# Kernel optimization log

Hardware: AMD Instinct MI355X
Metric: run time of the kernel (lower is better)

The kernel has to match this reference:

```python
import jax, jax.numpy as jnp
import numpy as np

N = 50000        # nodes
E = 800000       # directed edges (before self-loops)
F_IN = 128       # input node features
HID = 32         # hidden channels per head
HEADS = 4
NCLS = 8
EPS_BN = 1e-5
NEG_SLOPE = 0.2  # GATConv LeakyReLU default


def setup_inputs() -> dict:
    key = jax.random.key(0)
    ks = jax.random.split(key, 16)
    rn = lambda k, shape, s=0.1: jax.random.normal(k, shape, jnp.float32) * s
    inp = {}
    inp["x"] = jax.random.normal(ks[0], (N, F_IN), jnp.float32)
    inp["edge_index"] = jax.random.randint(ks[1], (2, E), 0, N, dtype=jnp.int32)
    # layer 0: F_IN -> HEADS*HID (concat)
    inp["W0"] = rn(ks[2], (F_IN, HEADS * HID))
    inp["as0"] = rn(ks[3], (HEADS, HID))
    inp["ad0"] = rn(ks[4], (HEADS, HID))
    inp["b0"] = jnp.zeros((HEADS * HID,), jnp.float32)
    inp["g0"] = jnp.ones((HEADS * HID,), jnp.float32)
    inp["bb0"] = jnp.zeros((HEADS * HID,), jnp.float32)
    inp["rm0"] = jnp.zeros((HEADS * HID,), jnp.float32)
    inp["rv0"] = jnp.ones((HEADS * HID,), jnp.float32)
    # layer 1: HEADS*HID -> HEADS*HID (concat)
    inp["W1"] = rn(ks[5], (HEADS * HID, HEADS * HID))
    inp["as1"] = rn(ks[6], (HEADS, HID))
    inp["ad1"] = rn(ks[7], (HEADS, HID))
    inp["b1"] = jnp.zeros((HEADS * HID,), jnp.float32)
    inp["g1"] = jnp.ones((HEADS * HID,), jnp.float32)
    inp["bb1"] = jnp.zeros((HEADS * HID,), jnp.float32)
    inp["rm1"] = jnp.zeros((HEADS * HID,), jnp.float32)
    inp["rv1"] = jnp.ones((HEADS * HID,), jnp.float32)
    # layer 2: HEADS*HID -> NCLS, heads=1, concat=False
    inp["W2"] = rn(ks[8], (HEADS * HID, NCLS))
    inp["as2"] = rn(ks[9], (1, NCLS))
    inp["ad2"] = rn(ks[10], (1, NCLS))
    inp["b2"] = jnp.zeros((NCLS,), jnp.float32)
    return inp


def gat_conv(x, src, dst, W, att_s, att_d, bias, H, C, concat):
    """PyG-style GATConv (eval mode, self-loops already appended to src/dst)."""
    n = x.shape[0]
    h = (x @ W).reshape(n, H, C)                       # [N,H,C]
    a_s = (h * att_s).sum(-1)                          # [N,H]
    a_d = (h * att_d).sum(-1)                          # [N,H]
    e = jax.nn.leaky_relu(a_s[src] + a_d[dst], NEG_SLOPE)  # [E,H]
    # numerically-stable segment softmax over incoming edges of each dst node
    m = jax.ops.segment_max(e, dst, num_segments=n)
    m = jnp.where(jnp.isfinite(m), m, 0.0)
    ex = jnp.exp(e - m[dst])
    den = jax.ops.segment_sum(ex, dst, num_segments=n)
    alpha = ex / (den[dst] + 1e-16)                    # [E,H]
    out = jax.ops.segment_sum(h[src] * alpha[:, :, None], dst, num_segments=n)  # [N,H,C]
    out = out.reshape(n, H * C) if concat else out.mean(axis=1)
    return out + bias


def bn_eval(x, g, b, rm, rv):
    return (x - rm) * jax.lax.rsqrt(rv + EPS_BN) * g + b


def reference(x, edge_index, W0, as0, ad0, b0, g0, bb0, rm0, rv0,
              W1, as1, ad1, b1, g1, bb1, rm1, rv1, W2, as2, ad2, b2):
    n = x.shape[0]
    loop = jnp.arange(n, dtype=edge_index.dtype)       # self-loops (PyG default)
    src = jnp.concatenate([edge_index[0], loop])
    dst = jnp.concatenate([edge_index[1], loop])
    h = gat_conv(x, src, dst, W0, as0, ad0, b0, HEADS, HID, True)
    h = jax.nn.elu(bn_eval(h, g0, bb0, rm0, rv0))
    h = gat_conv(h, src, dst, W1, as1, ad1, b1, HEADS, HID, True)
    h = jax.nn.elu(bn_eval(h, g1, bb1, rm1, rv1))
    h = gat_conv(h, src, dst, W2, as2, ad2, b2, 1, NCLS, False)
    return jax.nn.log_softmax(h, axis=1)
```

## Files before the change

### kernel.cpp

```cpp
#include <hip/hip_runtime.h>
#include <math.h>

#define N_NODES 50000
#define N_EDGES 800000
#define ET (N_EDGES + N_NODES)
#define FDIM 128
#define HEADS 4
#define HID 32
#define NCLS 8
#define NEG 0.2f
#define EPS_BN 1e-5f

#define BSH 6
#define NBUCK ((N_NODES + 63) >> BSH)
#define EPB 4096

typedef __attribute__((ext_vector_type(8))) short short8;
typedef __attribute__((ext_vector_type(4))) float f32x4;

__device__ __forceinline__ float lrelu(float e) { return e > 0.f ? e : NEG * e; }
__device__ __forceinline__ float bflo(unsigned u) { return __uint_as_float(u << 16); }
__device__ __forceinline__ float bfhi(unsigned u) { return __uint_as_float(u & 0xffff0000u); }
__device__ __forceinline__ unsigned f2bf(float f) {
    unsigned b = __float_as_uint(f);
    return (b + 0x7fffu + ((b >> 16) & 1u)) >> 16;
}

__device__ __forceinline__ void scan_bhist(const int* __restrict__ bhist,
                                           int* bloc, int* stmp) {
    int t = threadIdx.x;
    int idx = t * 4;
    int v0 = (idx     < NBUCK) ? bhist[idx]     : 0;
    int v1 = (idx + 1 < NBUCK) ? bhist[idx + 1] : 0;
    int v2 = (idx + 2 < NBUCK) ? bhist[idx + 2] : 0;
    int v3 = (idx + 3 < NBUCK) ? bhist[idx + 3] : 0;
    int sum = v0 + v1 + v2 + v3;
    stmp[t] = sum;
    __syncthreads();
    for (int off = 1; off < 256; off <<= 1) {
        int x = (t >= off) ? stmp[t - off] : 0;
        __syncthreads();
        stmp[t] += x;
        __syncthreads();
    }
    int run = stmp[t] - sum;
    if (idx     < NBUCK) bloc[idx]     = run; run += v0;
    if (idx + 1 < NBUCK) bloc[idx + 1] = run; run += v1;
    if (idx + 2 < NBUCK) bloc[idx + 2] = run; run += v2;
    if (idx + 3 < NBUCK) bloc[idx + 3] = run;
    __syncthreads();
}


#define CAST_B 3125
#define PACK_B 64
#define PB ((ET + EPB - 1) / EPB)

__global__ __launch_bounds__(256) void prep_hist(
        const float* __restrict__ x, unsigned short* __restrict__ xb,
        const float* __restrict__ W0, unsigned short* __restrict__ W0p,
        const float* __restrict__ W1, unsigned short* __restrict__ W1p,
        const int* __restrict__ ei, int* __restrict__ bhist) {
    __shared__ unsigned h[NBUCK];
    int b = blockIdx.x, tid = threadIdx.x;
    if (b < CAST_B) {
        int i = b * 256 + tid;
        const float4* p = (const float4*)x + (size_t)i * 2;
        float4 a = p[0], c = p[1];
        uint4 o;
        o.x = f2bf(a.x) | (f2bf(a.y) << 16);
        o.y = f2bf(a.z) | (f2bf(a.w) << 16);
        o.z = f2bf(c.x) | (f2bf(c.y) << 16);
        o.w = f2bf(c.z) | (f2bf(c.w) << 16);
        ((uint4*)xb)[i] = o;
    } else if (b < CAST_B + 2 * PACK_B) {
        int pb = b - CAST_B;
        const float* W = (pb < PACK_B) ? W0 : W1;
        unsigned short* Wp = (pb < PACK_B) ? W0p : W1p;
        int o = (pb & (PACK_B - 1)) * 256 + tid;
        int j = o & 7, lane = (o >> 3) & 63, kc = (o >> 9) & 3, t = o >> 11;
        int k = kc * 32 + ((lane >> 4) << 3) + j;
        int n = t * 16 + (lane & 15);
        Wp[o] = (unsigned short)f2bf(W[k * 128 + n]);
    } else {
        int blk = b - (CAST_B + 2 * PACK_B);
        int e0 = blk * EPB;
        for (int i = tid; i < NBUCK; i += 256) h[i] = 0;
        __syncthreads();
        #pragma unroll
        for (int k = 0; k < EPB / 256; k++) {
            int e = e0 + k * 256 + tid;
            if (e < ET) {
                int d = (e < N_EDGES) ? ei[N_EDGES + e] : (e - N_EDGES);
                atomicAdd(&h[d >> BSH], 1u);
            }
        }
        __syncthreads();
        for (int i = tid; i < NBUCK; i += 256)
            if (h[i]) atomicAdd(&bhist[i], (int)h[i]);
    }
}


__device__ __forceinline__ void gemm_attn_body(
        float* tiles, int gb,
        const unsigned short* __restrict__ Ab, const unsigned short* __restrict__ Wp,
        const float* __restrict__ att_s, const float* __restrict__ att_d,
        unsigned short* __restrict__ Hb, float* __restrict__ asn, float* __restrict__ adn,
        int M) {
    int tid = threadIdx.x;
    int wv = tid >> 6, lane = tid & 63;
    int base = gb * 64;
    int mrow = base + wv * 16 + (lane & 15);
    if (mrow >= M) mrow = M - 1;
    int koff = (lane >> 4) * 8;

    f32x4 acc[8];
    #pragma unroll
    for (int t = 0; t < 8; t++) acc[t] = (f32x4){0.f, 0.f, 0.f, 0.f};

    #pragma unroll
    for (int kc = 0; kc < 4; kc++) {
        short8 a = *(const short8*)(Ab + (size_t)mrow * 128 + kc * 32 + koff);
        #pragma unroll
        for (int t = 0; t < 8; t++) {
            short8 bfr = *(const short8*)(Wp + (((t * 4 + kc) * 64 + lane) << 3));
            acc[t] = __builtin_amdgcn_mfma_f32_16x16x32_bf16(a, bfr, acc[t], 0, 0, 0);
        }
    }

    int rbase = wv * 16 + (lane >> 4) * 4;
    int col = lane & 15;
    #pragma unroll
    for (int t = 0; t < 8; t++)
        #pragma unroll
        for (int r = 0; r < 4; r++)
            tiles[(rbase + r) * 132 + t * 16 + col] = acc[t][r];
    __syncthreads();

    #pragma unroll
    for (int it = 0; it < 4; it++) {
        int u = tid + it * 256;
        int rl = u >> 4, cg = u & 15;
        int row = base + rl;
        if (row < M) {
            const float* p = tiles + rl * 132 + cg * 8;
            float4 v0 = *(const float4*)(p);
            float4 v1 = *(const float4*)(p + 4);
            uint4 o;
            o.x = f2bf(v0.x) | (f2bf(v0.y) << 16);
            o.y = f2bf(v0.z) | (f2bf(v0.w) << 16);
            o.z = f2bf(v1.x) | (f2bf(v1.y) << 16);
            o.w = f2bf(v1.z) | (f2bf(v1.w) << 16);
            *(uint4*)(Hb + (size_t)row * 128 + cg * 8) = o;
        }
    }

    {
        int rl = tid >> 2, hd = tid & 3;
        int row = base + rl;
        if (row < M) {
            const float* hrow = tiles + rl * 132 + hd * 32;
            const float* as = att_s + hd * 32;
            const float* ad = att_d + hd * 32;
            float ps = 0.f, pd = 0.f;
            #pragma unroll
            for (int i = 0; i < 8; i++) {
                float4 hv = *(const float4*)(hrow + i * 4);
                float4 sv = *(const float4*)(as + i * 4);
                float4 dv = *(const float4*)(ad + i * 4);
                ps += hv.x * sv.x + hv.y * sv.y + hv.z * sv.z + hv.w * sv.w;
                pd += hv.x * dv.x + hv.y * dv.y + hv.z * dv.z + hv.w * dv.w;
            }
            asn[row * 4 + hd] = ps;
            adn[row * 4 + hd] = pd;
        }
    }
}


__global__ __launch_bounds__(256) void part_gemm(
        const int* __restrict__ ei, const int* __restrict__ bhist,
        int* __restrict__ bcur, int2* __restrict__ pairs,
        const unsigned short* __restrict__ Ab, const unsigned short* __restrict__ Wp,
        const float* __restrict__ att_s, const float* __restrict__ att_d,
        unsigned short* __restrict__ Hb, float* __restrict__ asn, float* __restrict__ adn,
        int M) {
    __shared__ float smem[64 * 132];
    int tid = threadIdx.x;
    if (blockIdx.x < PB) {
        unsigned* hist = (unsigned*)smem;
        unsigned* base = hist + NBUCK;
        int* bloc = (int*)(base + NBUCK);
        int* stmp = bloc + NBUCK;
        for (int i = tid; i < NBUCK; i += 256) hist[i] = 0;
        scan_bhist(bhist, bloc, stmp);
        int e0 = blockIdx.x * EPB;
        #pragma unroll
        for (int k = 0; k < EPB / 256; k++) {
            int e = e0 + k * 256 + tid;
            if (e < ET) {
                int d = (e < N_EDGES) ? ei[N_EDGES + e] : (e - N_EDGES);
                atomicAdd(&hist[d >> BSH], 1u);
            }
        }
        __syncthreads();
        for (int i = tid; i < NBUCK; i += 256) {
            unsigned h = hist[i];
            base[i] = h ? (unsigned)(bloc[i] + atomicAdd(&bcur[i], (int)h)) : 0u;
            hist[i] = 0;
        }
        __syncthreads();
        #pragma unroll
        for (int k = 0; k < EPB / 256; k++) {
            int e = e0 + k * 256 + tid;
            if (e < ET) {
                int s, d;
                if (e < N_EDGES) { s = ei[e]; d = ei[N_EDGES + e]; }
                else             { s = d = e - N_EDGES; }
                int bk = d >> BSH;
                unsigned lpos = atomicAdd(&hist[bk], 1u);
                pairs[base[bk] + lpos] = make_int2(s, d);
            }
        }
    } else {
        gemm_attn_body(smem, blockIdx.x - PB, Ab, Wp, att_s, att_d, Hb, asn, adn, M);
    }
}

__global__ __launch_bounds__(256) void gemm_attn(
        const unsigned short* __restrict__ Ab, const unsigned short* __restrict__ Wp,
        const float* __restrict__ att_s, const float* __restrict__ att_d,
        unsigned short* __restrict__ Hb, float* __restrict__ asn, float* __restrict__ adn,
        int M) {
    __shared__ float tiles[64 * 132];
    gemm_attn_body(tiles, blockIdx.x, Ab, Wp, att_s, att_d, Hb, asn, adn, M);
}


__global__ __launch_bounds__(256) void group_bucket(const int2* __restrict__ pairs,
                                                    const int* __restrict__ bhist,
                                                    int* __restrict__ offs,
                                                    int* __restrict__ ssrc) {
    __shared__ int bloc[NBUCK];
    __shared__ int stmp[256];
    __shared__ int cnt[64];
    int b = blockIdx.x, tid = threadIdx.x;
    scan_bhist(bhist, bloc, stmp);
    int base = bloc[b];
    int end = (b + 1 < NBUCK) ? bloc[b + 1] : ET;
    int n0 = b << BSH;
    if (tid < 64) cnt[tid] = 0;
    __syncthreads();
    for (int i = base + tid; i < end; i += 256)
        atomicAdd(&cnt[pairs[i].y & 63], 1);
    __syncthreads();
    int v = (tid < 64) ? cnt[tid] : 0;
    stmp[tid] = v;
    __syncthreads();
    for (int off = 1; off < 64; off <<= 1) {
        int x = (tid >= off) ? stmp[tid - off] : 0;
        __syncthreads();
        stmp[tid] += x;
        __syncthreads();
    }
    int excl = stmp[tid] - v;
    if (tid < 64) {
        if (n0 + tid < N_NODES) offs[n0 + tid] = base + excl;
        cnt[tid] = excl;
    }
    __syncthreads();
    for (int i = base + tid; i < end; i += 256) {
        int2 p = pairs[i];
        int pos = atomicAdd(&cnt[p.y & 63], 1);
        ssrc[base + pos] = p.x;
    }
    if (b == 0 && tid == 0) offs[N_NODES] = ET;
}


__global__ __launch_bounds__(256) void aggregate(
        const unsigned short* __restrict__ hb, const float* __restrict__ asn,
        const float* __restrict__ adn, const int* __restrict__ offs,
        const int* __restrict__ ssrc, const float* __restrict__ bias,
        const float* __restrict__ gamma, const float* __restrict__ beta,
        const float* __restrict__ rmean, const float* __restrict__ rvar,
        unsigned short* __restrict__ outb) {
    __shared__ int2 sPair[4][4][72];
    int wv = threadIdx.x >> 6;
    int node = blockIdx.x * 4 + wv;
    if (node >= N_NODES) return;
    int lane = threadIdx.x & 63;
    int hd = lane >> 4;
    int beg = offs[node], deg = offs[node + 1] - beg;
    float4 ad4 = *(const float4*)(adn + node * 4);

    if (lane < 32) sPair[wv][lane >> 3][64 + (lane & 7)] = make_int2(0, 0);

    float4 den4 = make_float4(0.f, 0.f, 0.f, 0.f);
    float acc0 = 0.f, acc1 = 0.f;
    const unsigned short* hlane = hb + 2 * lane;
    const int2* pp = &sPair[wv][hd][0];

    auto phaseC = [&](int cnt) {
        int bound = (cnt + 7) & ~7;
        for (int i = 0; i < bound; i += 8) {
            int2 p0 = pp[i],     p1 = pp[i + 1], p2 = pp[i + 2], p3 = pp[i + 3];
            int2 p4 = pp[i + 4], p5 = pp[i + 5], p6 = pp[i + 6], p7 = pp[i + 7];
            unsigned u0 = *(const unsigned*)(hlane + (((unsigned)p0.x) << 7));
            unsigned u1 = *(const unsigned*)(hlane + (((unsigned)p1.x) << 7));
            unsigned u2 = *(const unsigned*)(hlane + (((unsigned)p2.x) << 7));
            unsigned u3 = *(const unsigned*)(hlane + (((unsigned)p3.x) << 7));
            unsigned u4 = *(const unsigned*)(hlane + (((unsigned)p4.x) << 7));
            unsigned u5 = *(const unsigned*)(hlane + (((unsigned)p5.x) << 7));
            unsigned u6 = *(const unsigned*)(hlane + (((unsigned)p6.x) << 7));
            unsigned u7 = *(const unsigned*)(hlane + (((unsigned)p7.x) << 7));
            acc0 += __int_as_float(p0.y) * bflo(u0); acc1 += __int_as_float(p0.y) * bfhi(u0);
            acc0 += __int_as_float(p1.y) * bflo(u1); acc1 += __int_as_float(p1.y) * bfhi(u1);
            acc0 += __int_as_float(p2.y) * bflo(u2); acc1 += __int_as_float(p2.y) * bfhi(u2);
            acc0 += __int_as_float(p3.y) * bflo(u3); acc1 += __int_as_float(p3.y) * bfhi(u3);
            acc0 += __int_as_float(p4.y) * bflo(u4); acc1 += __int_as_float(p4.y) * bfhi(u4);
            acc0 += __int_as_float(p5.y) * bflo(u5); acc1 += __int_as_float(p5.y) * bfhi(u5);
            acc0 += __int_as_float(p6.y) * bflo(u6); acc1 += __int_as_float(p6.y) * bfhi(u6);
            acc0 += __int_as_float(p7.y) * bflo(u7); acc1 += __int_as_float(p7.y) * bfhi(u7);
        }
    };

    for (int base0 = 0; base0 < deg; base0 += 64) {
        int j = base0 + lane;
        int s = 0;
        float4 w4 = make_float4(0.f, 0.f, 0.f, 0.f);
        if (j < deg) {
            s = ssrc[beg + j];
            float4 a = *(const float4*)(asn + s * 4);
            w4.x = __expf(lrelu(a.x + ad4.x));
            w4.y = __expf(lrelu(a.y + ad4.y));
            w4.z = __expf(lrelu(a.z + ad4.z));
            w4.w = __expf(lrelu(a.w + ad4.w));
            den4.x += w4.x; den4.y += w4.y; den4.z += w4.z; den4.w += w4.w;
        }
        sPair[wv][0][lane] = make_int2(s, __float_as_int(w4.x));
        sPair[wv][1][lane] = make_int2(s, __float_as_int(w4.y));
        sPair[wv][2][lane] = make_int2(s, __float_as_int(w4.z));
        sPair[wv][3][lane] = make_int2(s, __float_as_int(w4.w));
        int cnt = deg - base0; if (cnt > 64) cnt = 64;
        phaseC(cnt);
    }

    #pragma unroll
    for (int off = 32; off; off >>= 1) {
        den4.x += __shfl_xor(den4.x, off);
        den4.y += __shfl_xor(den4.y, off);
        den4.z += __shfl_xor(den4.z, off);
        den4.w += __shfl_xor(den4.w, off);
    }
    float den = (hd & 2) ? ((hd & 1) ? den4.w : den4.z)
                         : ((hd & 1) ? den4.y : den4.x);
    float inv = 1.f / (den + 1e-16f);

    int c0 = lane * 2;
    float2 bi = *(const float2*)(bias + c0);
    float2 gm = *(const float2*)(gamma + c0);
    float2 bt = *(const float2*)(beta + c0);
    float2 rm = *(const float2*)(rmean + c0);
    float2 rv = *(const float2*)(rvar + c0);
    float o0 = acc0 * inv + bi.x;
    float o1 = acc1 * inv + bi.y;
    o0 = (o0 - rm.x) * rsqrtf(rv.x + EPS_BN) * gm.x + bt.x;
    o1 = (o1 - rm.y) * rsqrtf(rv.y + EPS_BN) * gm.y + bt.y;
    o0 = (o0 > 0.f) ? o0 : expm1f(o0);
    o1 = (o1 > 0.f) ? o1 : expm1f(o1);
    *(unsigned*)(outb + (size_t)node * 128 + c0) = f2bf(o0) | (f2bf(o1) << 16);
}


__global__ __launch_bounds__(256) void gemm2_fused(
        const unsigned short* __restrict__ xb, const float* __restrict__ W2,
        const float* __restrict__ as2, const float* __restrict__ ad2,
        float* __restrict__ h2, float* __restrict__ asn, float* __restrict__ adn) {
    __shared__ float sW[128 * 8];
    __shared__ float sas[8], sad[8];
    int tid = threadIdx.x;
    for (int i = tid; i < 1024; i += 256) sW[i] = W2[i];
    if (tid < 8) { sas[tid] = as2[tid]; sad[tid] = ad2[tid]; }
    __syncthreads();
    int node = blockIdx.x * 256 + tid;
    if (node >= N_NODES) return;
    const uint4* xr = (const uint4*)(xb + (size_t)node * 128);
    float acc[8];
    #pragma unroll
    for (int c = 0; c < 8; c++) acc[c] = 0.f;
    for (int k8 = 0; k8 < 16; k8++) {
        uint4 u = xr[k8];
        float f[8] = { bflo(u.x), bfhi(u.x), bflo(u.y), bfhi(u.y),
                       bflo(u.z), bfhi(u.z), bflo(u.w), bfhi(u.w) };
        int kb = k8 * 8;
        #pragma unroll
        for (int q = 0; q < 8; q++)
            #pragma unroll
            for (int c = 0; c < 8; c++)
                acc[c] += f[q] * sW[(kb + q) * 8 + c];
    }
    float ps = 0.f, pd = 0.f;
    #pragma unroll
    for (int c = 0; c < 8; c++) {
        h2[(size_t)node * 8 + c] = acc[c];
        ps += acc[c] * sas[c];
        pd += acc[c] * sad[c];
    }
    asn[node] = ps;
    adn[node] = pd;
}


__global__ __launch_bounds__(256) void aggregate2(
        const float* __restrict__ h2, const float* __restrict__ asn,
        const float* __restrict__ adn, const int* __restrict__ offs,
        const int* __restrict__ ssrc, const float* __restrict__ b2,
        float* __restrict__ out) {
    __shared__ int2 sPair[4][64];
    int wv = threadIdx.x >> 6;
    int node = blockIdx.x * 4 + wv;
    if (node >= N_NODES) return;
    int lane = threadIdx.x & 63;
    int g = lane >> 3, c = lane & 7;
    int beg = offs[node], end = offs[node + 1];
    int deg = end - beg;
    float adv = adn[node];

    float den = 0.f, acc = 0.f;
    auto phaseC = [&](int cnt) {
        int nIt = (cnt + 15) >> 4;
        const int2* pp = &sPair[wv][0];
        for (int i = 0; i < nIt; i++) {
            int e = i * 16 + g;
            int2 p0 = pp[e];
            int2 p1 = pp[e + 8];
            acc += __int_as_float(p0.y) * h2[(((unsigned)p0.x) << 3) + c];
            acc += __int_as_float(p1.y) * h2[(((unsigned)p1.x) << 3) + c];
        }
    };

    for (int base = 0; base < deg; base += 64) {
        int j = base + lane;
        int s = 0; float w = 0.f;
        if (j < deg) {
            s = ssrc[beg + j];
            w = __expf(lrelu(asn[s] + adv));
            den += w;
        }
        sPair[wv][lane] = make_int2(s, __float_as_int(w));
        int cnt = deg - base; if (cnt > 64) cnt = 64;
        phaseC(cnt);
    }

    acc += __shfl_xor(acc, 8); acc += __shfl_xor(acc, 16); acc += __shfl_xor(acc, 32);
    #pragma unroll
    for (int off = 32; off; off >>= 1) den += __shfl_xor(den, off);

    float o = acc / (den + 1e-16f) + b2[c];
    float mx = o;
    mx = fmaxf(mx, __shfl_xor(mx, 1));
    mx = fmaxf(mx, __shfl_xor(mx, 2));
    mx = fmaxf(mx, __shfl_xor(mx, 4));
    float ex = __expf(o - mx);
    float sm = ex;
    sm += __shfl_xor(sm, 1); sm += __shfl_xor(sm, 2); sm += __shfl_xor(sm, 4);
    if (g == 0) out[(size_t)node * 8 + c] = o - mx - logf(sm);
}


extern "C" void kernel_launch(void* const* d_in, const int* in_sizes, int n_in,
                              void* d_out, int out_size, void* d_ws, size_t ws_size,
                              hipStream_t stream) {
    const float* x   = (const float*)d_in[0];
    const int*   ei  = (const int*)d_in[1];
    const float* W0  = (const float*)d_in[2];
    const float* as0 = (const float*)d_in[3];
    const float* ad0 = (const float*)d_in[4];
    const float* b0  = (const float*)d_in[5];
    const float* g0  = (const float*)d_in[6];
    const float* bb0 = (const float*)d_in[7];
    const float* rm0 = (const float*)d_in[8];
    const float* rv0 = (const float*)d_in[9];
    const float* W1  = (const float*)d_in[10];
    const float* as1 = (const float*)d_in[11];
    const float* ad1 = (const float*)d_in[12];
    const float* b1  = (const float*)d_in[13];
    const float* g1  = (const float*)d_in[14];
    const float* bb1 = (const float*)d_in[15];
    const float* rm1 = (const float*)d_in[16];
    const float* rv1 = (const float*)d_in[17];
    const float* W2  = (const float*)d_in[18];
    const float* as2 = (const float*)d_in[19];
    const float* ad2 = (const float*)d_in[20];
    const float* b2  = (const float*)d_in[21];
    float* out = (float*)d_out;

    char* w = (char*)d_ws;
    size_t off = 0;
    auto carve = [&](size_t bytes) {
        void* p = w + off;
        off += (bytes + 255) & ~(size_t)255;
        return p;
    };
    unsigned short* xb   = (unsigned short*)carve((size_t)N_NODES * 128 * 2);
    unsigned short* Hb   = (unsigned short*)carve((size_t)N_NODES * 128 * 2);
    unsigned short* Xb   = (unsigned short*)carve((size_t)N_NODES * 128 * 2);
    unsigned short* W0p  = (unsigned short*)carve(16384 * 2);
    unsigned short* W1p  = (unsigned short*)carve(16384 * 2);
    int*   offs   = (int*)carve((size_t)(N_NODES + 1) * 4);
    int*   bhist  = (int*)carve((size_t)NBUCK * 2 * 4);
    int*   bcur   = bhist + NBUCK;
    int*   ssrc   = (int*)carve((size_t)ET * 4);
    int2*  pairs  = (int2*)carve((size_t)ET * 8);
    float* asn    = (float*)carve((size_t)N_NODES * 4 * 4);
    float* adn    = (float*)carve((size_t)N_NODES * 4 * 4);
    float* h2     = (float*)carve((size_t)N_NODES * 8 * 4);
    float* as2n   = (float*)carve((size_t)N_NODES * 4);
    float* ad2n   = (float*)carve((size_t)N_NODES * 4);
    (void)ws_size; (void)in_sizes; (void)n_in; (void)out_size;

    const int NB = (N_NODES + 255) / 256;
    const int GB = (N_NODES + 63) / 64;

    hipMemsetAsync(bhist, 0, (size_t)NBUCK * 2 * 4, stream);
    prep_hist<<<CAST_B + 2 * PACK_B + PB, 256, 0, stream>>>(x, xb, W0, W0p, W1, W1p, ei, bhist);
    part_gemm<<<PB + GB, 256, 0, stream>>>(ei, bhist, bcur, pairs,
                                           xb, W0p, as0, ad0, Hb, asn, adn, N_NODES);
    group_bucket<<<NBUCK, 256, 0, stream>>>(pairs, bhist, offs, ssrc);

    aggregate<<<(N_NODES + 3) / 4, 256, 0, stream>>>(Hb, asn, adn, offs, ssrc,
                                                     b0, g0, bb0, rm0, rv0, Xb);
    gemm_attn<<<GB, 256, 0, stream>>>(Xb, W1p, as1, ad1, Hb, asn, adn, N_NODES);
    aggregate<<<(N_NODES + 3) / 4, 256, 0, stream>>>(Hb, asn, adn, offs, ssrc,
                                                     b1, g1, bb1, rm1, rv1, Xb);
    gemm2_fused<<<NB, 256, 0, stream>>>(Xb, W2, as2, ad2, h2, as2n, ad2n);
    aggregate2<<<(N_NODES + 3) / 4, 256, 0, stream>>>(h2, as2n, ad2n, offs, ssrc, b2, out);
}
```

Before: 279.7 us.

## Fuse layer aggregation with following GEMM and attention projection

```diff
diff --git a/kernel.cpp b/kernel.cpp
--- a/kernel.cpp
+++ b/kernel.cpp
@@ -228,15 +228,6 @@
     }
 }
 
-__global__ __launch_bounds__(256) void gemm_attn(
-        const unsigned short* __restrict__ Ab, const unsigned short* __restrict__ Wp,
-        const float* __restrict__ att_s, const float* __restrict__ att_d,
-        unsigned short* __restrict__ Hb, float* __restrict__ asn, float* __restrict__ adn,
-        int M) {
-    __shared__ float tiles[64 * 132];
-    gemm_attn_body(tiles, blockIdx.x, Ab, Wp, att_s, att_d, Hb, asn, adn, M);
-}
-
 
 __global__ __launch_bounds__(256) void group_bucket(const int2* __restrict__ pairs,
                                                     const int* __restrict__ bhist,
@@ -279,13 +270,186 @@
 }
 
 
-__global__ __launch_bounds__(256) void aggregate(
+#define AGB 16
+#define NAGB (N_NODES / AGB)
+
+__global__ __launch_bounds__(256) void agg_gemm1(
         const unsigned short* __restrict__ hb, const float* __restrict__ asn,
         const float* __restrict__ adn, const int* __restrict__ offs,
         const int* __restrict__ ssrc, const float* __restrict__ bias,
         const float* __restrict__ gamma, const float* __restrict__ beta,
         const float* __restrict__ rmean, const float* __restrict__ rvar,
-        unsigned short* __restrict__ outb) {
+        const unsigned short* __restrict__ Wp,
+        const float* __restrict__ att_s, const float* __restrict__ att_d,
+        unsigned short* __restrict__ Hb2, float* __restrict__ asn1,
+        float* __restrict__ adn1) {
+    __shared__ __attribute__((aligned(16))) unsigned short At[16][136];
+    __shared__ __attribute__((aligned(16))) int2 sPair[4][4][72];
+    float* ftile = (float*)&sPair[0][0][0];
+
+    int tid = threadIdx.x;
+    int wv = tid >> 6, lane = tid & 63;
+    int hd = lane >> 4;
+    const unsigned short* hlane = hb + 2 * lane;
+    const int2* pp = &sPair[wv][hd][0];
+
+    if (lane < 32) sPair[wv][lane >> 3][64 + (lane & 7)] = make_int2(0, 0);
+
+    int c0 = lane * 2;
+    float2 bi = *(const float2*)(bias + c0);
+    float2 gm = *(const float2*)(gamma + c0);
+    float2 bt = *(const float2*)(beta + c0);
+    float2 rm = *(const float2*)(rmean + c0);
+    float2 rv = *(const float2*)(rvar + c0);
+    float sc0 = rsqrtf(rv.x + EPS_BN) * gm.x;
+    float sc1 = rsqrtf(rv.y + EPS_BN) * gm.y;
+
+    #pragma unroll 1
+    for (int q = 0; q < 4; q++) {
+        int lr = wv * 4 + q;
+        int node = blockIdx.x * AGB + lr;
+        int beg = offs[node], deg = offs[node + 1] - beg;
+        float4 ad4 = *(const float4*)(adn + node * 4);
+        float4 den4 = make_float4(0.f, 0.f, 0.f, 0.f);
+        float acc0 = 0.f, acc1 = 0.f;
+
+        auto phaseC = [&](int cnt) {
+            int bound = (cnt + 7) & ~7;
+            for (int i = 0; i < bound; i += 8) {
+                int2 p0 = pp[i],     p1 = pp[i + 1], p2 = pp[i + 2], p3 = pp[i + 3];
+                int2 p4 = pp[i + 4], p5 = pp[i + 5], p6 = pp[i + 6], p7 = pp[i + 7];
+                unsigned u0 = *(const unsigned*)(hlane + (((unsigned)p0.x) << 7));
+                unsigned u1 = *(const unsigned*)(hlane + (((unsigned)p1.x) << 7));
+                unsigned u2 = *(const unsigned*)(hlane + (((unsigned)p2.x) << 7));
+                unsigned u3 = *(const unsigned*)(hlane + (((unsigned)p3.x) << 7));
+                unsigned u4 = *(const unsigned*)(hlane + (((unsigned)p4.x) << 7));
+                unsigned u5 = *(const unsigned*)(hlane + (((unsigned)p5.x) << 7));
+                unsigned u6 = *(const unsigned*)(hlane + (((unsigned)p6.x) << 7));
+                unsigned u7 = *(const unsigned*)(hlane + (((unsigned)p7.x) << 7));
+                acc0 += __int_as_float(p0.y) * bflo(u0); acc1 += __int_as_float(p0.y) * bfhi(u0);
+                acc0 += __int_as_float(p1.y) * bflo(u1); acc1 += __int_as_float(p1.y) * bfhi(u1);
+                acc0 += __int_as_float(p2.y) * bflo(u2); acc1 += __int_as_float(p2.y) * bfhi(u2);
+                acc0 += __int_as_float(p3.y) * bflo(u3); acc1 += __int_as_float(p3.y) * bfhi(u3);
+                acc0 += __int_as_float(p4.y) * bflo(u4); acc1 += __int_as_float(p4.y) * bfhi(u4);
+                acc0 += __int_as_float(p5.y) * bflo(u5); acc1 += __int_as_float(p5.y) * bfhi(u5);
+                acc0 += __int_as_float(p6.y) * bflo(u6); acc1 += __int_as_float(p6.y) * bfhi(u6);
+                acc0 += __int_as_float(p7.y) * bflo(u7); acc1 += __int_as_float(p7.y) * bfhi(u7);
+            }
+        };
+
+        for (int base0 = 0; base0 < deg; base0 += 64) {
+            int j = base0 + lane;
+            int s = 0;
+            float4 w4 = make_float4(0.f, 0.f, 0.f, 0.f);
+            if (j < deg) {
+                s = ssrc[beg + j];
+                float4 a = *(const float4*)(asn + s * 4);
+                w4.x = __expf(lrelu(a.x + ad4.x));
+                w4.y = __expf(lrelu(a.y + ad4.y));
+                w4.z = __expf(lrelu(a.z + ad4.z));
+                w4.w = __expf(lrelu(a.w + ad4.w));
+                den4.x += w4.x; den4.y += w4.y; den4.z += w4.z; den4.w += w4.w;
+            }
+            sPair[wv][0][lane] = make_int2(s, __float_as_int(w4.x));
+            sPair[wv][1][lane] = make_int2(s, __float_as_int(w4.y));
+            sPair[wv][2][lane] = make_int2(s, __float_as_int(w4.z));
+            sPair[wv][3][lane] = make_int2(s, __float_as_int(w4.w));
+            int cnt = deg - base0; if (cnt > 64) cnt = 64;
+            phaseC(cnt);
+        }
+
+        #pragma unroll
+        for (int off = 32; off; off >>= 1) {
+            den4.x += __shfl_xor(den4.x, off);
+            den4.y += __shfl_xor(den4.y, off);
+            den4.z += __shfl_xor(den4.z, off);
+            den4.w += __shfl_xor(den4.w, off);
+        }
+        float den = (hd & 2) ? ((hd & 1) ? den4.w : den4.z)
+                             : ((hd & 1) ? den4.y : den4.x);
+        float inv = 1.f / (den + 1e-16f);
+
+        float o0 = acc0 * inv + bi.x;
+        float o1 = acc1 * inv + bi.y;
+        o0 = (o0 - rm.x) * sc0 + bt.x;
+        o1 = (o1 - rm.y) * sc1 + bt.y;
+        o0 = (o0 > 0.f) ? o0 : expm1f(o0);
+        o1 = (o1 > 0.f) ? o1 : expm1f(o1);
+        *(unsigned*)&At[lr][c0] = f2bf(o0) | (f2bf(o1) << 16);
+    }
+    __syncthreads();
+
+    int koff = hd * 8;
+    int ar = lane & 15;
+    f32x4 acc2[2];
+    acc2[0] = (f32x4){0.f, 0.f, 0.f, 0.f};
+    acc2[1] = (f32x4){0.f, 0.f, 0.f, 0.f};
+    #pragma unroll
+    for (int kc = 0; kc < 4; kc++) {
+        short8 a = *(const short8*)&At[ar][kc * 32 + koff];
+        #pragma unroll
+        for (int ti = 0; ti < 2; ti++) {
+            int t = wv * 2 + ti;
+            short8 bfr = *(const short8*)(Wp + (((t * 4 + kc) * 64 + lane) << 3));
+            acc2[ti] = __builtin_amdgcn_mfma_f32_16x16x32_bf16(a, bfr, acc2[ti], 0, 0, 0);
+        }
+    }
+    __syncthreads();
+
+    int rbase = hd * 4;
+    int col = lane & 15;
+    #pragma unroll
+    for (int ti = 0; ti < 2; ti++) {
+        int t = wv * 2 + ti;
+        #pragma unroll
+        for (int r = 0; r < 4; r++)
+            ftile[(rbase + r) * 132 + t * 16 + col] = acc2[ti][r];
+    }
+    __syncthreads();
+
+    {
+        int rl = tid >> 4, cg = tid & 15;
+        int row = blockIdx.x * AGB + rl;
+        const float* p = ftile + rl * 132 + cg * 8;
+        float4 v0 = *(const float4*)(p);
+        float4 v1 = *(const float4*)(p + 4);
+        uint4 o;
+        o.x = f2bf(v0.x) | (f2bf(v0.y) << 16);
+        o.y = f2bf(v0.z) | (f2bf(v0.w) << 16);
+        o.z = f2bf(v1.x) | (f2bf(v1.y) << 16);
+        o.w = f2bf(v1.z) | (f2bf(v1.w) << 16);
+        *(uint4*)(Hb2 + (size_t)row * 128 + cg * 8) = o;
+    }
+    if (tid < 64) {
+        int rl = tid >> 2, h2d = tid & 3;
+        int row = blockIdx.x * AGB + rl;
+        const float* hrow = ftile + rl * 132 + h2d * 32;
+        const float* as = att_s + h2d * 32;
+        const float* ad = att_d + h2d * 32;
+        float ps = 0.f, pd = 0.f;
+        #pragma unroll
+        for (int i = 0; i < 8; i++) {
+            float4 hv = *(const float4*)(hrow + i * 4);
+            float4 sv = *(const float4*)(as + i * 4);
+            float4 dv = *(const float4*)(ad + i * 4);
+            ps += hv.x * sv.x + hv.y * sv.y + hv.z * sv.z + hv.w * sv.w;
+            pd += hv.x * dv.x + hv.y * dv.y + hv.z * dv.z + hv.w * dv.w;
+        }
+        asn1[row * 4 + h2d] = ps;
+        adn1[row * 4 + h2d] = pd;
+    }
+}
+
+
+__global__ __launch_bounds__(256) void agg_mv2(
+        const unsigned short* __restrict__ hb, const float* __restrict__ asn,
+        const float* __restrict__ adn, const int* __restrict__ offs,
+        const int* __restrict__ ssrc, const float* __restrict__ bias,
+        const float* __restrict__ gamma, const float* __restrict__ beta,
+        const float* __restrict__ rmean, const float* __restrict__ rvar,
+        const float* __restrict__ W2, const float* __restrict__ as2,
+        const float* __restrict__ ad2, float* __restrict__ h2,
+        float* __restrict__ as2n, float* __restrict__ ad2n) {
     __shared__ int2 sPair[4][4][72];
     int wv = threadIdx.x >> 6;
     int node = blockIdx.x * 4 + wv;
@@ -370,46 +534,33 @@
     o1 = (o1 - rm.y) * rsqrtf(rv.y + EPS_BN) * gm.y + bt.y;
     o0 = (o0 > 0.f) ? o0 : expm1f(o0);
     o1 = (o1 > 0.f) ? o1 : expm1f(o1);
-    *(unsigned*)(outb + (size_t)node * 128 + c0) = f2bf(o0) | (f2bf(o1) << 16);
-}
-
-
-__global__ __launch_bounds__(256) void gemm2_fused(
-        const unsigned short* __restrict__ xb, const float* __restrict__ W2,
-        const float* __restrict__ as2, const float* __restrict__ ad2,
-        float* __restrict__ h2, float* __restrict__ asn, float* __restrict__ adn) {
-    __shared__ float sW[128 * 8];
-    __shared__ float sas[8], sad[8];
-    int tid = threadIdx.x;
-    for (int i = tid; i < 1024; i += 256) sW[i] = W2[i];
-    if (tid < 8) { sas[tid] = as2[tid]; sad[tid] = ad2[tid]; }
-    __syncthreads();
-    int node = blockIdx.x * 256 + tid;
-    if (node >= N_NODES) return;
-    const uint4* xr = (const uint4*)(xb + (size_t)node * 128);
-    float acc[8];
-    #pragma unroll
-    for (int c = 0; c < 8; c++) acc[c] = 0.f;
-    for (int k8 = 0; k8 < 16; k8++) {
-        uint4 u = xr[k8];
-        float f[8] = { bflo(u.x), bfhi(u.x), bflo(u.y), bfhi(u.y),
-                       bflo(u.z), bfhi(u.z), bflo(u.w), bfhi(u.w) };
-        int kb = k8 * 8;
-        #pragma unroll
-        for (int q = 0; q < 8; q++)
-            #pragma unroll
-            for (int c = 0; c < 8; c++)
-                acc[c] += f[q] * sW[(kb + q) * 8 + c];
-    }
-    float ps = 0.f, pd = 0.f;
-    #pragma unroll
-    for (int c = 0; c < 8; c++) {
-        h2[(size_t)node * 8 + c] = acc[c];
-        ps += acc[c] * sas[c];
-        pd += acc[c] * sad[c];
-    }
-    asn[node] = ps;
-    adn[node] = pd;
+
+    const float4* w2r = (const float4*)(W2 + c0 * 8);
+    float4 wa0 = w2r[0], wa1 = w2r[1], wb0 = w2r[2], wb1 = w2r[3];
+    float t8[8];
+    t8[0] = o0 * wa0.x + o1 * wb0.x;
+    t8[1] = o0 * wa0.y + o1 * wb0.y;
+    t8[2] = o0 * wa0.z + o1 * wb0.z;
+    t8[3] = o0 * wa0.w + o1 * wb0.w;
+    t8[4] = o0 * wa1.x + o1 * wb1.x;
+    t8[5] = o0 * wa1.y + o1 * wb1.y;
+    t8[6] = o0 * wa1.z + o1 * wb1.z;
+    t8[7] = o0 * wa1.w + o1 * wb1.w;
+    #pragma unroll
+    for (int off = 32; off; off >>= 1)
+        #pragma unroll
+        for (int c = 0; c < 8; c++) t8[c] += __shfl_xor(t8[c], off);
+    if (lane == 0) {
+        float ps = 0.f, pd = 0.f;
+        #pragma unroll
+        for (int c = 0; c < 8; c++) {
+            h2[(size_t)node * 8 + c] = t8[c];
+            ps += t8[c] * as2[c];
+            pd += t8[c] * ad2[c];
+        }
+        as2n[node] = ps;
+        ad2n[node] = pd;
+    }
 }
 
 
@@ -506,7 +657,7 @@
     };
     unsigned short* xb   = (unsigned short*)carve((size_t)N_NODES * 128 * 2);
     unsigned short* Hb   = (unsigned short*)carve((size_t)N_NODES * 128 * 2);
-    unsigned short* Xb   = (unsigned short*)carve((size_t)N_NODES * 128 * 2);
+    unsigned short* Hb2  = (unsigned short*)carve((size_t)N_NODES * 128 * 2);
     unsigned short* W0p  = (unsigned short*)carve(16384 * 2);
     unsigned short* W1p  = (unsigned short*)carve(16384 * 2);
     int*   offs   = (int*)carve((size_t)(N_NODES + 1) * 4);
@@ -514,27 +665,27 @@
     int*   bcur   = bhist + NBUCK;
     int*   ssrc   = (int*)carve((size_t)ET * 4);
     int2*  pairs  = (int2*)carve((size_t)ET * 8);
-    float* asn    = (float*)carve((size_t)N_NODES * 4 * 4);
-    float* adn    = (float*)carve((size_t)N_NODES * 4 * 4);
+    float* asn0   = (float*)carve((size_t)N_NODES * 4 * 4);
+    float* adn0   = (float*)carve((size_t)N_NODES * 4 * 4);
+    float* asn1   = (float*)carve((size_t)N_NODES * 4 * 4);
+    float* adn1   = (float*)carve((size_t)N_NODES * 4 * 4);
     float* h2     = (float*)carve((size_t)N_NODES * 8 * 4);
     float* as2n   = (float*)carve((size_t)N_NODES * 4);
     float* ad2n   = (float*)carve((size_t)N_NODES * 4);
     (void)ws_size; (void)in_sizes; (void)n_in; (void)out_size;
 
-    const int NB = (N_NODES + 255) / 256;
     const int GB = (N_NODES + 63) / 64;
 
     hipMemsetAsync(bhist, 0, (size_t)NBUCK * 2 * 4, stream);
     prep_hist<<<CAST_B + 2 * PACK_B + PB, 256, 0, stream>>>(x, xb, W0, W0p, W1, W1p, ei, bhist);
     part_gemm<<<PB + GB, 256, 0, stream>>>(ei, bhist, bcur, pairs,
-                                           xb, W0p, as0, ad0, Hb, asn, adn, N_NODES);
+                                           xb, W0p, as0, ad0, Hb, asn0, adn0, N_NODES);
     group_bucket<<<NBUCK, 256, 0, stream>>>(pairs, bhist, offs, ssrc);
-
-    aggregate<<<(N_NODES + 3) / 4, 256, 0, stream>>>(Hb, asn, adn, offs, ssrc,
-                                                     b0, g0, bb0, rm0, rv0, Xb);
-    gemm_attn<<<GB, 256, 0, stream>>>(Xb, W1p, as1, ad1, Hb, asn, adn, N_NODES);
-    aggregate<<<(N_NODES + 3) / 4, 256, 0, stream>>>(Hb, asn, adn, offs, ssrc,
-                                                     b1, g1, bb1, rm1, rv1, Xb);
-    gemm2_fused<<<NB, 256, 0, stream>>>(Xb, W2, as2, ad2, h2, as2n, ad2n);
+    agg_gemm1<<<NAGB, 256, 0, stream>>>(Hb, asn0, adn0, offs, ssrc,
+                                        b0, g0, bb0, rm0, rv0,
+                                        W1p, as1, ad1, Hb2, asn1, adn1);
+    agg_mv2<<<(N_NODES + 3) / 4, 256, 0, stream>>>(Hb2, asn1, adn1, offs, ssrc,
+                                                   b1, g1, bb1, rm1, rv1,
+                                                   W2, as2, ad2, h2, as2n, ad2n);
     aggregate2<<<(N_NODES + 3) / 4, 256, 0, stream>>>(h2, as2n, ad2n, offs, ssrc, b2, out);
 }
```

New measurement: 279.7 us. No clear change (+0.0%).
